# Kernel optimization log

Hardware: AMD Instinct MI355X
Metric: run time of the kernel (lower is better)

The kernel has to match this reference:

```python
import jax, jax.numpy as jnp
import numpy as np
import math

D_MODEL = 512
N_HEADS = 8
D_K = D_MODEL // N_HEADS
B, N = 2, 2048


def setup_inputs() -> dict:
    key = jax.random.key(0)
    ks = jax.random.split(key, 13)
    s = 1.0 / math.sqrt(D_MODEL)
    inp = {
        "x": jax.random.normal(ks[0], (B, N, D_MODEL), dtype=jnp.float32),
        "D": jax.random.uniform(ks[1], (B, N, N), dtype=jnp.float32),
        "A": jax.random.uniform(ks[2], (B, N, N), dtype=jnp.float32),
        "Wq": jax.random.normal(ks[3], (D_MODEL, D_MODEL), dtype=jnp.float32) * s,
        "bq": jnp.zeros((D_MODEL,), dtype=jnp.float32),
        "Wk": jax.random.normal(ks[4], (D_MODEL, D_MODEL), dtype=jnp.float32) * s,
        "bk": jnp.zeros((D_MODEL,), dtype=jnp.float32),
        "Wv": jax.random.normal(ks[5], (D_MODEL, D_MODEL), dtype=jnp.float32) * s,
        "bv": jnp.zeros((D_MODEL,), dtype=jnp.float32),
        "Wo": jax.random.normal(ks[6], (D_MODEL, D_MODEL), dtype=jnp.float32) * s,
        "bo": jnp.zeros((D_MODEL,), dtype=jnp.float32),
        # learned per-head bias scalars; init nonzero so biases matter numerically
        "w_d": jax.random.normal(ks[7], (1, N_HEADS, 1, 1), dtype=jnp.float32) * 0.1,
        "w_a": jax.random.normal(ks[8], (1, N_HEADS, 1, 1), dtype=jnp.float32) * 0.1,
    }
    return inp


def reference(x, D, A, Wq, bq, Wk, bk, Wv, bv, Wo, bo, w_d, w_a):
    b, n, _ = x.shape
    # project and split heads: (B, H, N, d_k)
    def heads(W, bias):
        return (x @ W.T + bias).reshape(b, n, N_HEADS, D_K).transpose(0, 2, 1, 3)
    q = heads(Wq, bq)
    k = heads(Wk, bk)
    v = heads(Wv, bv)
    scale = 1.0 / math.sqrt(D_K)
    # (B, H, N, N) scores with learned-scalar-weighted tree biases
    scores = jnp.einsum("bhqd,bhkd->bhqk", q, k) * scale
    scores = scores + w_d * D[:, None, :, :] + w_a * A[:, None, :, :]
    attn = jax.nn.softmax(scores, axis=-1)
    out = jnp.einsum("bhqk,bhkd->bhqd", attn, v)
    out = out.transpose(0, 2, 1, 3).reshape(b, n, D_MODEL)
    return out @ Wo.T + bo
```

## Files before the change

### kernel.cpp

```cpp
#include <hip/hip_runtime.h>
#include <hip/hip_bf16.h>
#include <math.h>

typedef unsigned short ushort_t;
typedef unsigned int   uint_t;
typedef __attribute__((ext_vector_type(8))) short  bf16x8;
typedef __attribute__((ext_vector_type(4))) float  f32x4;
typedef __attribute__((ext_vector_type(4))) int    int4v;
typedef __attribute__((ext_vector_type(4))) short  s16x4;

#define MFMA16(a, b, c) __builtin_amdgcn_mfma_f32_16x16x32_bf16((a), (b), (c), 0, 0, 0)

static constexpr int BATCH = 2;
static constexpr int SEQ   = 2048;
static constexpr int DMODEL = 512;
static constexpr int NHEADS = 8;
static constexpr int DK    = 64;
static constexpr int MROWS = BATCH * SEQ;
static constexpr int XE = MROWS * DMODEL;
static constexpr int WE = DMODEL * DMODEL;
static constexpr int NQKV = 3 * DMODEL;
static constexpr int NSPLIT = 4;
static constexpr int KB_PER = (SEQ / 64) / NSPLIT;

__device__ __forceinline__ ushort_t f2bf(float f) {
  unsigned int u = __builtin_bit_cast(unsigned int, f);
  u = (u + 0x7FFFu + ((u >> 16) & 1u)) >> 16;
  return (ushort_t)u;
}

__device__ __forceinline__ void async16(const ushort_t* g, ushort_t* l) {
  __builtin_amdgcn_global_load_lds(
      (const __attribute__((address_space(1))) unsigned int*)g,
      (__attribute__((address_space(3))) unsigned int*)l, 16, 0, 0);
}

__global__ __launch_bounds__(256) void convert_kernel(
    const float* __restrict__ x,  const float* __restrict__ wq,
    const float* __restrict__ wk, const float* __restrict__ wv,
    const float* __restrict__ wo,
    const float* __restrict__ bq, const float* __restrict__ bk,
    const float* __restrict__ bv,
    ushort_t* __restrict__ dst, float* __restrict__ bqkv) {
  const int bid = blockIdx.x;
  if (bid == (XE + 4 * WE) / 1024) {
    for (int i = threadIdx.x; i < NQKV; i += 256) {
      bqkv[i] = (i < 512) ? bq[i] : (i < 1024) ? bk[i - 512] : bv[i - 1024];
    }
    return;
  }
  int e = (bid * 256 + threadIdx.x) * 4;
  const float* src;
  int off;
  if (e < XE)                { src = x;  off = e; }
  else if (e < XE + WE)      { src = wq; off = e - XE; }
  else if (e < XE + 2 * WE)  { src = wk; off = e - XE - WE; }
  else if (e < XE + 3 * WE)  { src = wv; off = e - XE - 2 * WE; }
  else                       { src = wo; off = e - XE - 3 * WE; }
  float4 f = *reinterpret_cast<const float4*>(&src[off]);
  s16x4 v;
  v[0] = (short)f2bf(f.x); v[1] = (short)f2bf(f.y);
  v[2] = (short)f2bf(f.z); v[3] = (short)f2bf(f.w);
  *reinterpret_cast<s16x4*>(&dst[e]) = v;
}

__global__ __launch_bounds__(256) void pack_da_kernel(
    const float* __restrict__ Dm, const float* __restrict__ Am,
    uint_t* __restrict__ out) {
  int e = (blockIdx.x * 256 + threadIdx.x) * 4;
  float4 d = *reinterpret_cast<const float4*>(&Dm[e]);
  float4 a = *reinterpret_cast<const float4*>(&Am[e]);
  int4v v;
  v[0] = (int)((uint_t)f2bf(d.x) | ((uint_t)f2bf(a.x) << 16));
  v[1] = (int)((uint_t)f2bf(d.y) | ((uint_t)f2bf(a.y) << 16));
  v[2] = (int)((uint_t)f2bf(d.z) | ((uint_t)f2bf(a.z) << 16));
  v[3] = (int)((uint_t)f2bf(d.w) | ((uint_t)f2bf(a.w) << 16));
  *reinterpret_cast<int4v*>(&out[e]) = v;
}

template <bool F32OUT>
__global__ __launch_bounds__(256) void gemm_bt(
    const ushort_t* __restrict__ A, const ushort_t* __restrict__ Bt,
    const float* __restrict__ bias, void* __restrict__ C,
    int N, int K) {
  __shared__ ushort_t As[64][64];
  __shared__ ushort_t Bs[64][64];
  const int tid  = threadIdx.x;
  const int wave = tid >> 6, lane = tid & 63;
  const int quad = lane >> 4, l15 = lane & 15;
  const int m0 = blockIdx.y * 64, n0 = blockIdx.x * 64;

  f32x4 acc[4] = {};

  const int lrow = lane >> 3, slot = lane & 7;
  const int cswz = 8 * (slot ^ lrow);
  const ushort_t* ag = A  + (size_t)(m0 + wave * 16 + lrow) * K + cswz;
  const ushort_t* bg = Bt + (size_t)(n0 + wave * 16 + lrow) * K + cswz;
  ushort_t* la0 = &As[wave * 16][0];
  ushort_t* la1 = &As[wave * 16 + 8][0];
  ushort_t* lb0 = &Bs[wave * 16][0];
  ushort_t* lb1 = &Bs[wave * 16 + 8][0];

  const int swz = l15 & 7;

  for (int k0 = 0; k0 < K; k0 += 64) {
    __syncthreads();
    async16(ag + k0, la0);
    async16(ag + k0 + 8 * (size_t)K, la1);
    async16(bg + k0, lb0);
    async16(bg + k0 + 8 * (size_t)K, lb1);
    asm volatile("s_waitcnt vmcnt(0)" ::: "memory");
    __syncthreads();
#pragma unroll
    for (int s = 0; s < 2; s++) {
      const int acol = 8 * ((s * 4 + quad) ^ swz);
      bf16x8 af = *reinterpret_cast<const bf16x8*>(&As[wave * 16 + l15][acol]);
#pragma unroll
      for (int t = 0; t < 4; t++) {
        bf16x8 bfr = *reinterpret_cast<const bf16x8*>(&Bs[t * 16 + l15][acol]);
        acc[t] = MFMA16(af, bfr, acc[t]);
      }
    }
  }

#pragma unroll
  for (int t = 0; t < 4; t++) {
    const int col = n0 + t * 16 + l15;
    const float bv = bias[col];
#pragma unroll
    for (int rr = 0; rr < 4; rr++) {
      const int row = m0 + wave * 16 + quad * 4 + rr;
      const float v = acc[t][rr] + bv;
      if (F32OUT) reinterpret_cast<float*>(C)[(size_t)row * N + col] = v;
      else        reinterpret_cast<ushort_t*>(C)[(size_t)row * N + col] = f2bf(v);
    }
  }
}

__global__ __launch_bounds__(256) void attn_kernel(
    const ushort_t* __restrict__ QKV, const uint_t* __restrict__ DA,
    const float* __restrict__ wd, const float* __restrict__ wa,
    float* __restrict__ Opart, float* __restrict__ Mp, float* __restrict__ Lp) {
  const int qb = blockIdx.x, h = blockIdx.y;
  const int b = blockIdx.z / NSPLIT, split = blockIdx.z % NSPLIT;
  const int tid = threadIdx.x;
  const int wave = tid >> 6, lane = tid & 63;
  const int quad = lane >> 4, l15 = lane & 15;
  const int q0 = qb * 64;
  const float scale = 0.125f;
  const float wdh = wd[h], wah = wa[h];

  __shared__ ushort_t Ks[64][64];
  __shared__ ushort_t Vts[64][64];
  __shared__ ushort_t Ps[4][16][72];

  const int qrow = q0 + wave * 16 + l15;
  bf16x8 qf[2];
#pragma unroll
  for (int s = 0; s < 2; s++)
    qf[s] = *reinterpret_cast<const bf16x8*>(
        &QKV[(size_t)(b * SEQ + qrow) * NQKV + h * DK + s * 32 + quad * 8]);

  float m_run[4], l_run[4];
  f32x4 o[4] = {};
#pragma unroll
  for (int rr = 0; rr < 4; rr++) { m_run[rr] = -INFINITY; l_run[rr] = 0.f; }

  const int lrow = lane >> 3, slot = lane & 7;
  const ushort_t* kg = QKV + (size_t)(b * SEQ + wave * 16 + lrow) * NQKV +
                       512 + h * DK + 8 * (slot ^ lrow);
  ushort_t* lk0 = &Ks[wave * 16][0];
  ushort_t* lk1 = &Ks[wave * 16 + 8][0];

  const int sr = tid >> 3;
  const int sc = (tid & 7) * 8;
  const int c7 = tid & 7;
  const ushort_t* vg = QKV + (size_t)(b * SEQ + sr) * NQKV + 1024 + h * DK + sc;
  const int col0 = (sr & 7) + 8 * ((sr >> 3) ^ c7);
  const int col1 = (sr & 7) + 8 * (((sr >> 3) + 4) ^ c7);

  const int swz = l15 & 7;
  const uint_t* DArow = DA + (size_t)b * SEQ * SEQ;

  for (int kbi = 0; kbi < KB_PER; kbi++) {
    const int k0 = (split * KB_PER + kbi) * 64;
    __syncthreads();
    async16(kg + (size_t)k0 * NQKV, lk0);
    async16(kg + (size_t)(k0 + 8) * NQKV, lk1);
    bf16x8 v0 = *reinterpret_cast<const bf16x8*>(vg + (size_t)k0 * NQKV);
    bf16x8 v1 = *reinterpret_cast<const bf16x8*>(vg + (size_t)(k0 + 32) * NQKV);
#pragma unroll
    for (int j = 0; j < 8; j++) {
      Vts[sc + j][col0] = (ushort_t)v0[j];
      Vts[sc + j][col1] = (ushort_t)v1[j];
    }
    asm volatile("s_waitcnt vmcnt(0)" ::: "memory");
    __syncthreads();

    uint_t da[4][4];
#pragma unroll
    for (int t = 0; t < 4; t++) {
      const int kk = k0 + t * 16 + l15;
#pragma unroll
      for (int rr = 0; rr < 4; rr++) {
        const int qg = q0 + wave * 16 + quad * 4 + rr;
        da[t][rr] = DArow[(size_t)qg * SEQ + kk];
      }
    }

    f32x4 sacc[4];
#pragma unroll
    for (int t = 0; t < 4; t++) {
      bf16x8 kf0 = *reinterpret_cast<const bf16x8*>(&Ks[t * 16 + l15][8 * (quad ^ swz)]);
      bf16x8 kf1 = *reinterpret_cast<const bf16x8*>(&Ks[t * 16 + l15][8 * ((4 + quad) ^ swz)]);
      f32x4 z = {};
      z = MFMA16(qf[0], kf0, z);
      sacc[t] = MFMA16(qf[1], kf1, z);
    }

    float sv[4][4];
    float mx[4] = {-INFINITY, -INFINITY, -INFINITY, -INFINITY};
#pragma unroll
    for (int t = 0; t < 4; t++) {
#pragma unroll
      for (int rr = 0; rr < 4; rr++) {
        const float fd = __builtin_bit_cast(float, da[t][rr] << 16);
        const float fa = __builtin_bit_cast(float, da[t][rr] & 0xFFFF0000u);
        float s = fmaf(wdh, fd, fmaf(wah, fa, sacc[t][rr] * scale));
        sv[t][rr] = s;
        mx[rr] = fmaxf(mx[rr], s);
      }
    }
#pragma unroll
    for (int rr = 0; rr < 4; rr++) {
      float m = mx[rr];
#pragma unroll
      for (int off = 1; off < 16; off <<= 1) m = fmaxf(m, __shfl_xor(m, off, 64));
      mx[rr] = m;
    }
    float alpha[4], rs[4];
#pragma unroll
    for (int rr = 0; rr < 4; rr++) {
      const float mn = fmaxf(m_run[rr], mx[rr]);
      alpha[rr] = __expf(m_run[rr] - mn);
      m_run[rr] = mn;
      rs[rr] = 0.f;
    }
#pragma unroll
    for (int t = 0; t < 4; t++) {
#pragma unroll
      for (int rr = 0; rr < 4; rr++) {
        const float p = __expf(sv[t][rr] - m_run[rr]);
        rs[rr] += p;
        Ps[wave][quad * 4 + rr][t * 16 + l15] = f2bf(p);
      }
    }
#pragma unroll
    for (int rr = 0; rr < 4; rr++) {
      float s = rs[rr];
#pragma unroll
      for (int off = 1; off < 16; off <<= 1) s += __shfl_xor(s, off, 64);
      l_run[rr] = l_run[rr] * alpha[rr] + s;
    }
#pragma unroll
    for (int dt = 0; dt < 4; dt++)
#pragma unroll
      for (int rr = 0; rr < 4; rr++) o[dt][rr] *= alpha[rr];

    asm volatile("s_waitcnt lgkmcnt(0)" ::: "memory");

#pragma unroll
    for (int s2 = 0; s2 < 2; s2++) {
      bf16x8 pf = *reinterpret_cast<const bf16x8*>(&Ps[wave][l15][s2 * 32 + quad * 8]);
#pragma unroll
      for (int dt = 0; dt < 4; dt++) {
        const int vrow = dt * 16 + l15;
        const int vcb = (s2 * 4 + quad) ^ (vrow >> 3);
        bf16x8 vf = *reinterpret_cast<const bf16x8*>(&Vts[vrow][vcb * 8]);
        o[dt] = MFMA16(pf, vf, o[dt]);
      }
    }
  }

  const int pidx = (((b * NHEADS + h) * 32 + qb) * NSPLIT + split);
  float* op = Opart + (size_t)pidx * 4096;
#pragma unroll
  for (int dt = 0; dt < 4; dt++) {
#pragma unroll
    for (int rr = 0; rr < 4; rr++) {
      const int row = wave * 16 + quad * 4 + rr;
      op[row * 64 + dt * 16 + l15] = o[dt][rr];
    }
  }
  if (l15 == 0) {
#pragma unroll
    for (int rr = 0; rr < 4; rr++) {
      const int row = wave * 16 + quad * 4 + rr;
      Mp[(size_t)pidx * 64 + row] = m_run[rr];
      Lp[(size_t)pidx * 64 + row] = l_run[rr];
    }
  }
}

__global__ __launch_bounds__(256) void combine_kernel(
    const float* __restrict__ Opart, const float* __restrict__ Mp,
    const float* __restrict__ Lp, ushort_t* __restrict__ AO) {
  const int qb = blockIdx.x, h = blockIdx.y, b = blockIdx.z;
  const int tid = threadIdx.x;
  const int lane = tid & 63, wq = tid >> 6;
  const int pidx0 = ((b * NHEADS + h) * 32 + qb) * NSPLIT;

  for (int r = 0; r < 16; r++) {
    const int q = wq * 16 + r;
    float m[NSPLIT], l[NSPLIT];
    float M = -INFINITY;
#pragma unroll
    for (int s = 0; s < NSPLIT; s++) {
      m[s] = Mp[(size_t)(pidx0 + s) * 64 + q];
      l[s] = Lp[(size_t)(pidx0 + s) * 64 + q];
      M = fmaxf(M, m[s]);
    }
    float L = 0.f, acc = 0.f;
#pragma unroll
    for (int s = 0; s < NSPLIT; s++) {
      const float w = __expf(m[s] - M);
      L += l[s] * w;
      acc += Opart[(size_t)(pidx0 + s) * 4096 + q * 64 + lane] * w;
    }
    const int row = b * SEQ + qb * 64 + q;
    AO[(size_t)row * DMODEL + h * DK + lane] = f2bf(acc / L);
  }
}

extern "C" void kernel_launch(void* const* d_in, const int* in_sizes, int n_in,
                              void* d_out, int out_size, void* d_ws, size_t ws_size,
                              hipStream_t stream) {
  const float* x  = (const float*)d_in[0];
  const float* Dm = (const float*)d_in[1];
  const float* Am = (const float*)d_in[2];
  const float* Wq = (const float*)d_in[3];
  const float* bq = (const float*)d_in[4];
  const float* Wk = (const float*)d_in[5];
  const float* bk = (const float*)d_in[6];
  const float* Wv = (const float*)d_in[7];
  const float* bv = (const float*)d_in[8];
  const float* Wo = (const float*)d_in[9];
  const float* bo = (const float*)d_in[10];
  const float* wd = (const float*)d_in[11];
  const float* wa = (const float*)d_in[12];

  char* ws = (char*)d_ws;
  size_t off = 0;
  ushort_t* xb    = (ushort_t*)(ws + off); off += (size_t)XE * 2;
  ushort_t* wqkvb = (ushort_t*)(ws + off); off += (size_t)3 * WE * 2;
  ushort_t* wob   = (ushort_t*)(ws + off); off += (size_t)WE * 2;
  ushort_t* QKVb  = (ushort_t*)(ws + off); off += (size_t)MROWS * NQKV * 2;
  ushort_t* AO    = (ushort_t*)(ws + off); off += (size_t)XE * 2;
  float*    bqkv  = (float*)(ws + off);    off += (size_t)NQKV * 4;
  off = (off + 255) & ~(size_t)255;
  uint_t*   DAb   = (uint_t*)(ws + off);   off += (size_t)BATCH * SEQ * SEQ * 4;
  float*    Opart = (float*)(ws + off);    off += (size_t)512 * NSPLIT * 4096 * 4;
  float*    Mpart = (float*)(ws + off);    off += (size_t)512 * NSPLIT * 64 * 4;
  float*    Lpart = (float*)(ws + off);

  const int conv_blocks = (XE + 4 * WE) / 1024;
  convert_kernel<<<conv_blocks + 1, 256, 0, stream>>>(
      x, Wq, Wk, Wv, Wo, bq, bk, bv, xb, bqkv);
  pack_da_kernel<<<(BATCH * SEQ * SEQ) / 1024, 256, 0, stream>>>(Dm, Am, DAb);

  dim3 qkvgrid(NQKV / 64, MROWS / 64);
  gemm_bt<false><<<qkvgrid, 256, 0, stream>>>(xb, wqkvb, bqkv, QKVb, NQKV, DMODEL);

  dim3 agrid(SEQ / 64, NHEADS, BATCH * NSPLIT);
  attn_kernel<<<agrid, 256, 0, stream>>>(QKVb, DAb, wd, wa, Opart, Mpart, Lpart);
  dim3 cgrid(SEQ / 64, NHEADS, BATCH);
  combine_kernel<<<cgrid, 256, 0, stream>>>(Opart, Mpart, Lpart, AO);

  dim3 ogrid(DMODEL / 64, MROWS / 64);
  gemm_bt<true><<<ogrid, 256, 0, stream>>>(AO, wob, bo, (float*)d_out, DMODEL, DMODEL);
}
```

Before: 237.3 us.

## Fold softmax scale into Wq, use exp2, lazy rescale, MFMA row sums

Folds the 1/sqrt(dk)·log2e factor into the bf16 Q weights and bias, and the log2e factor into the per-head bias scalars, so the attention kernel can use the raw v_exp_f32 (exp2) directly. It replaces shuffle-based row max with DPP reductions and computes row sums through an extra MFMA against a ones vector instead of shuffles. Rescaling of the running output is skipped unless some row's max grows past a threshold, which trades exactness of the running max for less work per tile. It also permutes the P store layout and the V load mapping, and uses packed bf16 conversion to write P with a single vector store.

```diff
diff --git a/kernel.cpp b/kernel.cpp
--- a/kernel.cpp
+++ b/kernel.cpp
@@ -7,6 +7,7 @@
 typedef __attribute__((ext_vector_type(8))) short  bf16x8;
 typedef __attribute__((ext_vector_type(4))) float  f32x4;
 typedef __attribute__((ext_vector_type(4))) int    int4v;
+typedef __attribute__((ext_vector_type(2))) int    i32x2;
 typedef __attribute__((ext_vector_type(4))) short  s16x4;
 
 #define MFMA16(a, b, c) __builtin_amdgcn_mfma_f32_16x16x32_bf16((a), (b), (c), 0, 0, 0)
@@ -23,10 +24,38 @@
 static constexpr int NSPLIT = 4;
 static constexpr int KB_PER = (SEQ / 64) / NSPLIT;
 
+static constexpr float QSCALE_L2E = 0.18033688011112043f;
+static constexpr float L2E = 1.4426950408889634f;
+
 __device__ __forceinline__ ushort_t f2bf(float f) {
   unsigned int u = __builtin_bit_cast(unsigned int, f);
   u = (u + 0x7FFFu + ((u >> 16) & 1u)) >> 16;
   return (ushort_t)u;
+}
+
+__device__ __forceinline__ float fexp2(float x) {
+  float r;
+  asm("v_exp_f32 %0, %1" : "=v"(r) : "v"(x));
+  return r;
+}
+
+__device__ __forceinline__ int cvt_pk_bf16(float a, float b) {
+  int r;
+  asm("v_cvt_pk_bf16_f32 %0, %1, %2" : "=v"(r) : "v"(a), "v"(b));
+  return r;
+}
+
+__device__ __forceinline__ float rowmax16(float x) {
+  int t;
+  t = __builtin_amdgcn_mov_dpp(__builtin_bit_cast(int, x), 0xB1, 0xF, 0xF, true);
+  x = fmaxf(x, __builtin_bit_cast(float, t));
+  t = __builtin_amdgcn_mov_dpp(__builtin_bit_cast(int, x), 0x4E, 0xF, 0xF, true);
+  x = fmaxf(x, __builtin_bit_cast(float, t));
+  t = __builtin_amdgcn_mov_dpp(__builtin_bit_cast(int, x), 0x141, 0xF, 0xF, true);
+  x = fmaxf(x, __builtin_bit_cast(float, t));
+  t = __builtin_amdgcn_mov_dpp(__builtin_bit_cast(int, x), 0x140, 0xF, 0xF, true);
+  x = fmaxf(x, __builtin_bit_cast(float, t));
+  return x;
 }
 
 __device__ __forceinline__ void async16(const ushort_t* g, ushort_t* l) {
@@ -45,22 +74,24 @@
   const int bid = blockIdx.x;
   if (bid == (XE + 4 * WE) / 1024) {
     for (int i = threadIdx.x; i < NQKV; i += 256) {
-      bqkv[i] = (i < 512) ? bq[i] : (i < 1024) ? bk[i - 512] : bv[i - 1024];
+      bqkv[i] = (i < 512) ? bq[i] * QSCALE_L2E
+              : (i < 1024) ? bk[i - 512] : bv[i - 1024];
     }
     return;
   }
   int e = (bid * 256 + threadIdx.x) * 4;
   const float* src;
   int off;
+  float qs = 1.0f;
   if (e < XE)                { src = x;  off = e; }
-  else if (e < XE + WE)      { src = wq; off = e - XE; }
+  else if (e < XE + WE)      { src = wq; off = e - XE; qs = QSCALE_L2E; }
   else if (e < XE + 2 * WE)  { src = wk; off = e - XE - WE; }
   else if (e < XE + 3 * WE)  { src = wv; off = e - XE - 2 * WE; }
   else                       { src = wo; off = e - XE - 3 * WE; }
   float4 f = *reinterpret_cast<const float4*>(&src[off]);
   s16x4 v;
-  v[0] = (short)f2bf(f.x); v[1] = (short)f2bf(f.y);
-  v[2] = (short)f2bf(f.z); v[3] = (short)f2bf(f.w);
+  v[0] = (short)f2bf(f.x * qs); v[1] = (short)f2bf(f.y * qs);
+  v[2] = (short)f2bf(f.z * qs); v[3] = (short)f2bf(f.w * qs);
   *reinterpret_cast<s16x4*>(&dst[e]) = v;
 }
 
@@ -147,12 +178,11 @@
   const int wave = tid >> 6, lane = tid & 63;
   const int quad = lane >> 4, l15 = lane & 15;
   const int q0 = qb * 64;
-  const float scale = 0.125f;
-  const float wdh = wd[h], wah = wa[h];
+  const float wdh = wd[h] * L2E, wah = wa[h] * L2E;
 
   __shared__ ushort_t Ks[64][64];
   __shared__ ushort_t Vts[64][64];
-  __shared__ ushort_t Ps[4][16][72];
+  __shared__ __align__(16) ushort_t Ps[4][16][72];
 
   const int qrow = q0 + wave * 16 + l15;
   bf16x8 qf[2];
@@ -160,6 +190,10 @@
   for (int s = 0; s < 2; s++)
     qf[s] = *reinterpret_cast<const bf16x8*>(
         &QKV[(size_t)(b * SEQ + qrow) * NQKV + h * DK + s * 32 + quad * 8]);
+
+  bf16x8 ones;
+#pragma unroll
+  for (int j = 0; j < 8; j++) ones[j] = (short)0x3F80;
 
   float m_run[4], l_run[4];
   f32x4 o[4] = {};
@@ -172,15 +206,21 @@
   ushort_t* lk0 = &Ks[wave * 16][0];
   ushort_t* lk1 = &Ks[wave * 16 + 8][0];
 
-  const int sr = tid >> 3;
-  const int sc = (tid & 7) * 8;
+  const int u  = tid >> 3;
   const int c7 = tid & 7;
-  const ushort_t* vg = QKV + (size_t)(b * SEQ + sr) * NQKV + 1024 + h * DK + sc;
-  const int col0 = (sr & 7) + 8 * ((sr >> 3) ^ c7);
-  const int col1 = (sr & 7) + 8 * (((sr >> 3) + 4) ^ c7);
+  const int sc = c7 * 8;
+  const int kv = ((u & 3) << 4) | (u >> 2);
+  const ushort_t* vg = QKV + (size_t)(b * SEQ + kv) * NQKV + 1024 + h * DK + sc;
+  const int col0 = (u & 7) + 8 * ((u >> 3) ^ c7);
+  const int col1 = (u & 7) + 8 * (((u >> 3) + 4) ^ c7);
 
   const int swz = l15 & 7;
-  const uint_t* DArow = DA + (size_t)b * SEQ * SEQ;
+
+  const uint_t* dap[4];
+#pragma unroll
+  for (int rr = 0; rr < 4; rr++)
+    dap[rr] = DA + (size_t)b * SEQ * SEQ +
+              (size_t)(q0 + wave * 16 + quad * 4 + rr) * SEQ + l15;
 
   for (int kbi = 0; kbi < KB_PER; kbi++) {
     const int k0 = (split * KB_PER + kbi) * 64;
@@ -188,7 +228,7 @@
     async16(kg + (size_t)k0 * NQKV, lk0);
     async16(kg + (size_t)(k0 + 8) * NQKV, lk1);
     bf16x8 v0 = *reinterpret_cast<const bf16x8*>(vg + (size_t)k0 * NQKV);
-    bf16x8 v1 = *reinterpret_cast<const bf16x8*>(vg + (size_t)(k0 + 32) * NQKV);
+    bf16x8 v1 = *reinterpret_cast<const bf16x8*>(vg + (size_t)(k0 + 8) * NQKV);
 #pragma unroll
     for (int j = 0; j < 8; j++) {
       Vts[sc + j][col0] = (ushort_t)v0[j];
@@ -200,12 +240,8 @@
     uint_t da[4][4];
 #pragma unroll
     for (int t = 0; t < 4; t++) {
-      const int kk = k0 + t * 16 + l15;
-#pragma unroll
-      for (int rr = 0; rr < 4; rr++) {
-        const int qg = q0 + wave * 16 + quad * 4 + rr;
-        da[t][rr] = DArow[(size_t)qg * SEQ + kk];
-      }
+#pragma unroll
+      for (int rr = 0; rr < 4; rr++) da[t][rr] = dap[rr][k0 + t * 16];
     }
 
     f32x4 sacc[4];
@@ -226,49 +262,44 @@
       for (int rr = 0; rr < 4; rr++) {
         const float fd = __builtin_bit_cast(float, da[t][rr] << 16);
         const float fa = __builtin_bit_cast(float, da[t][rr] & 0xFFFF0000u);
-        float s = fmaf(wdh, fd, fmaf(wah, fa, sacc[t][rr] * scale));
+        float s = fmaf(wdh, fd, fmaf(wah, fa, sacc[t][rr]));
         sv[t][rr] = s;
         mx[rr] = fmaxf(mx[rr], s);
       }
     }
 #pragma unroll
+    for (int rr = 0; rr < 4; rr++) mx[rr] = rowmax16(mx[rr]);
+
+    bool grow = false;
+#pragma unroll
+    for (int rr = 0; rr < 4; rr++) grow |= (mx[rr] > m_run[rr] + 11.5f);
+    if (__ballot(grow)) {
+      float alpha[4];
+#pragma unroll
+      for (int rr = 0; rr < 4; rr++) {
+        const float mn = fmaxf(m_run[rr], mx[rr]);
+        alpha[rr] = fexp2(m_run[rr] - mn);
+        m_run[rr] = mn;
+        l_run[rr] *= alpha[rr];
+      }
+#pragma unroll
+      for (int dt = 0; dt < 4; dt++)
+#pragma unroll
+        for (int rr = 0; rr < 4; rr++) o[dt][rr] *= alpha[rr];
+    }
+
+#pragma unroll
     for (int rr = 0; rr < 4; rr++) {
-      float m = mx[rr];
-#pragma unroll
-      for (int off = 1; off < 16; off <<= 1) m = fmaxf(m, __shfl_xor(m, off, 64));
-      mx[rr] = m;
-    }
-    float alpha[4], rs[4];
-#pragma unroll
-    for (int rr = 0; rr < 4; rr++) {
-      const float mn = fmaxf(m_run[rr], mx[rr]);
-      alpha[rr] = __expf(m_run[rr] - mn);
-      m_run[rr] = mn;
-      rs[rr] = 0.f;
-    }
-#pragma unroll
-    for (int t = 0; t < 4; t++) {
-#pragma unroll
-      for (int rr = 0; rr < 4; rr++) {
-        const float p = __expf(sv[t][rr] - m_run[rr]);
-        rs[rr] += p;
-        Ps[wave][quad * 4 + rr][t * 16 + l15] = f2bf(p);
-      }
-    }
-#pragma unroll
-    for (int rr = 0; rr < 4; rr++) {
-      float s = rs[rr];
-#pragma unroll
-      for (int off = 1; off < 16; off <<= 1) s += __shfl_xor(s, off, 64);
-      l_run[rr] = l_run[rr] * alpha[rr] + s;
-    }
-#pragma unroll
-    for (int dt = 0; dt < 4; dt++)
-#pragma unroll
-      for (int rr = 0; rr < 4; rr++) o[dt][rr] *= alpha[rr];
+      const float m = m_run[rr];
+      i32x2 w;
+      w[0] = cvt_pk_bf16(fexp2(sv[0][rr] - m), fexp2(sv[1][rr] - m));
+      w[1] = cvt_pk_bf16(fexp2(sv[2][rr] - m), fexp2(sv[3][rr] - m));
+      *reinterpret_cast<i32x2*>(&Ps[wave][quad * 4 + rr][l15 * 4]) = w;
+    }
 
     asm volatile("s_waitcnt lgkmcnt(0)" ::: "memory");
 
+    f32x4 rsacc = {};
 #pragma unroll
     for (int s2 = 0; s2 < 2; s2++) {
       bf16x8 pf = *reinterpret_cast<const bf16x8*>(&Ps[wave][l15][s2 * 32 + quad * 8]);
@@ -279,7 +310,10 @@
         bf16x8 vf = *reinterpret_cast<const bf16x8*>(&Vts[vrow][vcb * 8]);
         o[dt] = MFMA16(pf, vf, o[dt]);
       }
-    }
+      rsacc = MFMA16(pf, ones, rsacc);
+    }
+#pragma unroll
+    for (int rr = 0; rr < 4; rr++) l_run[rr] += rsacc[rr];
   }
 
   const int pidx = (((b * NHEADS + h) * 32 + qb) * NSPLIT + split);
@@ -323,7 +357,7 @@
     float L = 0.f, acc = 0.f;
 #pragma unroll
     for (int s = 0; s < NSPLIT; s++) {
-      const float w = __expf(m[s] - M);
+      const float w = fexp2(m[s] - M);
       L += l[s] * w;
       acc += Opart[(size_t)(pidx0 + s) * 4096 + q * 64 + lane] * w;
     }
```

After: 226.9 us. 1.05x faster.
